# Kernel tuning notes

Hardware: AMD Instinct MI355X
Metric: run time of the kernel (lower is better)

Reference implementation:

```python
import jax, jax.numpy as jnp
import numpy as np

EPS = 1e-5

def fwht(x):
    """Normalized fast Walsh-Hadamard transform along the last axis (len must be power of 2)."""
    orig_shape = x.shape
    n = orig_shape[-1]
    x = x.reshape(-1, n)
    h = 1
    while h < n:
        x = x.reshape(-1, n // (2 * h), 2, h)
        a, b = x[:, :, 0, :], x[:, :, 1, :]
        x = jnp.stack([a + b, a - b], axis=2).reshape(-1, n)
        h *= 2
    return (x * (1.0 / np.sqrt(n))).reshape(orig_shape)

def act_quant(x):
    """Per-token 8-bit absmax activation quantization (BitNet), with STE identity."""
    scale = 127.0 / jnp.clip(jnp.max(jnp.abs(x), axis=-1, keepdims=True), EPS)
    q = jnp.clip(jnp.round(x * scale), -128.0, 127.0) / scale
    return x + jax.lax.stop_gradient(q - x)

def weight_quant(w):
    """Ternary (1.58-bit) absmean weight quantization (BitNet b1.58), with STE identity."""
    scale = jnp.clip(jnp.mean(jnp.abs(w)), EPS)
    q = jnp.clip(jnp.round(w / scale), -1.0, 1.0) * scale
    return w + jax.lax.stop_gradient(q - w)

def h_bitlinear(x, w):
    """EnhancedHBitLinear: Hadamard-rotate activations, quantize acts+weights, matmul."""
    xq = act_quant(fwht(x))
    wq = weight_quant(w)
    return jnp.einsum('bsh,oh->bso', xq, wq)

def setup_inputs() -> dict:
    key = jax.random.key(0)
    k1, k2, k3, k4 = jax.random.split(key, 4)
    H, I = 2048, 8192
    B, S = 2, 2048
    hidden_states = jax.random.normal(k1, (B, S, H), dtype=jnp.float32)
    w_gate = jax.random.normal(k2, (I, H), dtype=jnp.float32) * 0.02
    w_up = jax.random.normal(k3, (I, H), dtype=jnp.float32) * 0.02
    w_down = jax.random.normal(k4, (H, I), dtype=jnp.float32) * 0.02
    return {"hidden_states": hidden_states, "w_gate": w_gate, "w_up": w_up, "w_down": w_down}

def reference(hidden_states, w_gate, w_up, w_down):
    gate = h_bitlinear(hidden_states, w_gate)          # [B,S,I]
    up = h_bitlinear(hidden_states, w_up)              # [B,S,I]
    return h_bitlinear(jax.nn.silu(gate) * up, w_down)  # [B,S,H]
```

## Files before the change

### kernel.cpp

```cpp
#include <hip/hip_runtime.h>
#include <math.h>

#define EPSF 1e-5f

typedef __attribute__((ext_vector_type(4))) int i32x4;

#define S_WAITCNT_VMCNT(N) asm volatile("s_waitcnt vmcnt(" #N ")" ::: "memory")
#define S_WAITCNT_LGKM0() asm volatile("s_waitcnt lgkmcnt(0)" ::: "memory")

__device__ __forceinline__ void gload_lds16(const void* g, void* l) {
  __builtin_amdgcn_global_load_lds(
      (const __attribute__((address_space(1))) void*)g,
      (__attribute__((address_space(3))) void*)l, 16, 0, 0);
}

__global__ void zero_sums_kernel(double* sums) {
  if (threadIdx.x < 3) sums[threadIdx.x] = 0.0;
}

__global__ __launch_bounds__(256) void absmean_kernel(
    const float* __restrict__ wg, const float* __restrict__ wu,
    const float* __restrict__ wd, double* __restrict__ sums) {
  const int N4 = 16777216 / 4;
  const float* W = (blockIdx.y == 0) ? wg : ((blockIdx.y == 1) ? wu : wd);
  double acc = 0.0;
  const int stride = gridDim.x * 256;
  for (int i = blockIdx.x * 256 + threadIdx.x; i < N4; i += stride) {
    float4 v = ((const float4*)W)[i];
    acc += (double)fabsf(v.x);
    acc += (double)fabsf(v.y);
    acc += (double)fabsf(v.z);
    acc += (double)fabsf(v.w);
  }
  for (int o = 32; o > 0; o >>= 1) acc += __shfl_down(acc, o);
  __shared__ double sred[4];
  const int wid = threadIdx.x >> 6, lane = threadIdx.x & 63;
  if (lane == 0) sred[wid] = acc;
  __syncthreads();
  if (threadIdx.x == 0)
    atomicAdd(&sums[blockIdx.y], sred[0] + sred[1] + sred[2] + sred[3]);
}

__global__ __launch_bounds__(256) void wquant_kernel(
    const float* __restrict__ wg, const float* __restrict__ wu,
    const float* __restrict__ wd, signed char* __restrict__ qg,
    signed char* __restrict__ qu, signed char* __restrict__ qd,
    const double* __restrict__ sums, float* __restrict__ scalef) {
  const int mat = blockIdx.y;
  const float* W = (mat == 0) ? wg : ((mat == 1) ? wu : wd);
  signed char* Q = (mat == 0) ? qg : ((mat == 1) ? qu : qd);
  const float scale = fmaxf((float)(sums[mat] * (1.0 / 16777216.0)), EPSF);
  if (blockIdx.x == 0 && threadIdx.x == 0) scalef[mat] = scale;
  const int i = blockIdx.x * 256 + threadIdx.x;
  float4 v = ((const float4*)W)[i];
  int q0 = (int)fminf(fmaxf(rintf(v.x / scale), -1.f), 1.f);
  int q1 = (int)fminf(fmaxf(rintf(v.y / scale), -1.f), 1.f);
  int q2 = (int)fminf(fmaxf(rintf(v.z / scale), -1.f), 1.f);
  int q3 = (int)fminf(fmaxf(rintf(v.w / scale), -1.f), 1.f);
  int packed = (q0 & 0xff) | ((q1 & 0xff) << 8) | ((q2 & 0xff) << 16) | (q3 << 24);
  ((int*)Q)[i] = packed;
}

template <int N>
__global__ __launch_bounds__(256) void fwht_quant_kernel(
    const float* __restrict__ X, signed char* __restrict__ Q,
    float* __restrict__ drow, float cnorm) {
  __shared__ float s[N];
  __shared__ float red[4];
  const int tid = threadIdx.x;
  const size_t row = blockIdx.x;
  const float* x = X + row * (size_t)N;
  for (int i = tid; i < N / 4; i += 256)
    ((float4*)s)[i] = ((const float4*)x)[i];
  __syncthreads();
  for (int h = 1; h < N; h <<= 1) {
    for (int p = tid; p < N / 2; p += 256) {
      int i = ((p & ~(h - 1)) << 1) | (p & (h - 1));
      int j = i + h;
      float a = s[i], b = s[j];
      s[i] = a + b;
      s[j] = a - b;
    }
    __syncthreads();
  }
  const int PER = N / 256;
  float m = 0.f;
  for (int i = tid * PER; i < tid * PER + PER; ++i) m = fmaxf(m, fabsf(s[i]));
  for (int o = 32; o > 0; o >>= 1) m = fmaxf(m, __shfl_xor(m, o));
  const int wid = tid >> 6, lane = tid & 63;
  if (lane == 0) red[wid] = m;
  __syncthreads();
  m = fmaxf(fmaxf(red[0], red[1]), fmaxf(red[2], red[3]));
  const float maxv = fmaxf(m * cnorm, EPSF);
  const float scale = 127.0f / maxv;
  if (tid == 0) drow[row] = maxv / 127.0f;
  const size_t qbase = row * (size_t)N + (size_t)tid * PER;
#pragma unroll
  for (int i0 = 0; i0 < PER; i0 += 4) {
    int q[4];
#pragma unroll
    for (int k = 0; k < 4; ++k) {
      float y = s[tid * PER + i0 + k] * cnorm;
      float qf = rintf(y * scale);
      qf = fminf(fmaxf(qf, -128.f), 127.f);
      q[k] = (int)qf;
    }
    int packed =
        (q[0] & 0xff) | ((q[1] & 0xff) << 8) | ((q[2] & 0xff) << 16) | (q[3] << 24);
    *(int*)(Q + qbase + i0) = packed;
  }
}

__global__ __launch_bounds__(256, 2) void gemm1_kernel(
    const signed char* __restrict__ Aq, const signed char* __restrict__ Bg,
    const signed char* __restrict__ Bu, const float* __restrict__ drow,
    const float* __restrict__ scalef, float* __restrict__ H) {
  const int K = 2048, T = K / 64;
  const int BUF = 24576;
  __shared__ __align__(16) signed char smem[3 * BUF];
  const int tid = threadIdx.x;
  const int wid = tid >> 6;
  const int lane = tid & 63;
  const int wr = wid >> 1, wc = wid & 1;

  const int orig = blockIdx.y * 64 + blockIdx.x;
  const int swz = (orig & 7) * 256 + (orig >> 3);
  const int mbase = (swz >> 6) * 128, nbase = (swz & 63) * 128;

  const int srow = tid >> 2;
  const int scol = (((tid & 3) ^ ((srow >> 1) & 3)) << 4);
  const signed char* gA = Aq + (size_t)(mbase + srow) * K + scol;
  const signed char* gG = Bg + (size_t)(nbase + srow) * K + scol;
  const signed char* gU = Bu + (size_t)(nbase + srow) * K + scol;

  i32x4 accG[4][4] = {};
  i32x4 accU[4][4] = {};

  auto stage = [&](int boff, int kk) {
    const size_t o = (size_t)kk;
    const int lb = boff + (wid << 10);
    gload_lds16(gA + o, &smem[lb]);
    gload_lds16(gA + o + (size_t)64 * K, &smem[lb + 4096]);
    gload_lds16(gG + o, &smem[lb + 8192]);
    gload_lds16(gG + o + (size_t)64 * K, &smem[lb + 12288]);
    gload_lds16(gU + o, &smem[lb + 16384]);
    gload_lds16(gU + o + (size_t)64 * K, &smem[lb + 20480]);
  };

  const int kos = (((lane >> 4) ^ ((lane >> 1) & 3)) << 4);
  const int rA = (wr << 6) + (lane & 15);
  const int rB = (wc << 6) + (lane & 15);

  stage(0, 0);
  stage(BUF, 64);
  int bc = 0, bn = BUF, bf = 2 * BUF;
  for (int t = 0; t < T; ++t) {
    S_WAITCNT_VMCNT(6);
    __builtin_amdgcn_s_barrier();
    __builtin_amdgcn_sched_barrier(0);
    const int kk = (t + 2 < T) ? (t + 2) * 64 : (T - 1) * 64;
    stage(bf, kk);
    i32x4 a[4], bg[4], bu[4];
#pragma unroll
    for (int m = 0; m < 4; ++m)
      a[m] = *(const i32x4*)&smem[bc + (rA + m * 16) * 64 + kos];
#pragma unroll
    for (int n = 0; n < 4; ++n) {
      bg[n] = *(const i32x4*)&smem[bc + 8192 + (rB + n * 16) * 64 + kos];
      bu[n] = *(const i32x4*)&smem[bc + 16384 + (rB + n * 16) * 64 + kos];
    }
    __builtin_amdgcn_s_setprio(1);
#pragma unroll
    for (int m = 0; m < 4; ++m)
#pragma unroll
      for (int n = 0; n < 4; ++n) {
        accG[m][n] =
            __builtin_amdgcn_mfma_i32_16x16x64_i8(a[m], bg[n], accG[m][n], 0, 0, 0);
        accU[m][n] =
            __builtin_amdgcn_mfma_i32_16x16x64_i8(a[m], bu[n], accU[m][n], 0, 0, 0);
      }
    __builtin_amdgcn_s_setprio(0);
    S_WAITCNT_LGKM0();
    __builtin_amdgcn_sched_barrier(0);
    const int tmp = bc; bc = bn; bn = bf; bf = tmp;
  }

  const float sg = scalef[0], su = scalef[1];
  const int orow = (lane >> 4) << 2;
  const int ocol = lane & 15;
#pragma unroll
  for (int m = 0; m < 4; ++m)
#pragma unroll
    for (int n = 0; n < 4; ++n)
#pragma unroll
      for (int j = 0; j < 4; ++j) {
        int grow = mbase + (wr << 6) + m * 16 + orow + j;
        int gcol = nbase + (wc << 6) + n * 16 + ocol;
        float dr = drow[grow];
        float gate = (float)accG[m][n][j] * (sg * dr);
        float up = (float)accU[m][n][j] * (su * dr);
        float hval = (gate / (1.0f + expf(-gate))) * up;
        H[(size_t)grow * 8192 + gcol] = hval;
      }
}

__global__ __launch_bounds__(256, 3) void gemm2_kernel(
    const signed char* __restrict__ Aq, const signed char* __restrict__ Bq,
    const float* __restrict__ drow, const float* __restrict__ scalef,
    float* __restrict__ O) {
  const int K = 8192, T = K / 64;
  const int BUF = 16384;
  __shared__ __align__(16) signed char smem[3 * BUF];
  const int tid = threadIdx.x;
  const int wid = tid >> 6;
  const int lane = tid & 63;
  const int wr = wid >> 1, wc = wid & 1;

  const int orig = blockIdx.y * 16 + blockIdx.x;
  const int swz = (orig & 7) * 64 + (orig >> 3);
  const int mbase = (swz >> 4) * 128, nbase = (swz & 15) * 128;

  const int srow = tid >> 2;
  const int scol = (((tid & 3) ^ ((srow >> 1) & 3)) << 4);
  const signed char* gA = Aq + (size_t)(mbase + srow) * K + scol;
  const signed char* gB = Bq + (size_t)(nbase + srow) * K + scol;

  i32x4 acc[4][4] = {};

  auto stage = [&](int boff, int kk) {
    const size_t o = (size_t)kk;
    const int lb = boff + (wid << 10);
    gload_lds16(gA + o, &smem[lb]);
    gload_lds16(gA + o + (size_t)64 * K, &smem[lb + 4096]);
    gload_lds16(gB + o, &smem[lb + 8192]);
    gload_lds16(gB + o + (size_t)64 * K, &smem[lb + 12288]);
  };

  const int kos = (((lane >> 4) ^ ((lane >> 1) & 3)) << 4);
  const int rA = (wr << 6) + (lane & 15);
  const int rB = (wc << 6) + (lane & 15);

  stage(0, 0);
  stage(BUF, 64);
  int bc = 0, bn = BUF, bf = 2 * BUF;
  for (int t = 0; t < T; ++t) {
    S_WAITCNT_VMCNT(4);
    __builtin_amdgcn_s_barrier();
    __builtin_amdgcn_sched_barrier(0);
    const int kk = (t + 2 < T) ? (t + 2) * 64 : (T - 1) * 64;
    stage(bf, kk);
    i32x4 a[4], b[4];
#pragma unroll
    for (int m = 0; m < 4; ++m)
      a[m] = *(const i32x4*)&smem[bc + (rA + m * 16) * 64 + kos];
#pragma unroll
    for (int n = 0; n < 4; ++n)
      b[n] = *(const i32x4*)&smem[bc + 8192 + (rB + n * 16) * 64 + kos];
    __builtin_amdgcn_s_setprio(1);
#pragma unroll
    for (int m = 0; m < 4; ++m)
#pragma unroll
      for (int n = 0; n < 4; ++n)
        acc[m][n] = __builtin_amdgcn_mfma_i32_16x16x64_i8(a[m], b[n], acc[m][n], 0, 0, 0);
    __builtin_amdgcn_s_setprio(0);
    S_WAITCNT_LGKM0();
    __builtin_amdgcn_sched_barrier(0);
    const int tmp = bc; bc = bn; bn = bf; bf = tmp;
  }

  const float sd = scalef[2];
  const int orow = (lane >> 4) << 2;
  const int ocol = lane & 15;
#pragma unroll
  for (int m = 0; m < 4; ++m)
#pragma unroll
    for (int n = 0; n < 4; ++n)
#pragma unroll
      for (int j = 0; j < 4; ++j) {
        int grow = mbase + (wr << 6) + m * 16 + orow + j;
        int gcol = nbase + (wc << 6) + n * 16 + ocol;
        O[(size_t)grow * 2048 + gcol] = (float)acc[m][n][j] * (sd * drow[grow]);
      }
}

extern "C" void kernel_launch(void* const* d_in, const int* in_sizes, int n_in,
                              void* d_out, int out_size, void* d_ws, size_t ws_size,
                              hipStream_t stream) {
  (void)in_sizes; (void)n_in; (void)out_size; (void)ws_size;
  const float* x = (const float*)d_in[0];
  const float* wg = (const float*)d_in[1];
  const float* wu = (const float*)d_in[2];
  const float* wd = (const float*)d_in[3];
  float* out = (float*)d_out;

  char* ws = (char*)d_ws;
  double* sums = (double*)ws;
  float* scalef = (float*)(ws + 256);
  size_t off = 1024;
  signed char* qg = (signed char*)(ws + off); off += 16777216;
  signed char* qu = (signed char*)(ws + off); off += 16777216;
  signed char* qd = (signed char*)(ws + off); off += 16777216;
  signed char* xq = (signed char*)(ws + off); off += 8388608;
  signed char* hq = (signed char*)(ws + off); off += 33554432;
  float* dr1 = (float*)(ws + off); off += 16384;
  float* dr2 = (float*)(ws + off); off += 16384;
  float* Hbuf = (float*)(ws + off); off += (size_t)4096 * 8192 * 4;

  zero_sums_kernel<<<1, 64, 0, stream>>>(sums);
  absmean_kernel<<<dim3(1024, 3), 256, 0, stream>>>(wg, wu, wd, sums);
  wquant_kernel<<<dim3(16384, 3), 256, 0, stream>>>(wg, wu, wd, qg, qu, qd, sums,
                                                    scalef);
  const float c1 = (float)(1.0 / sqrt(2048.0));
  const float c2 = (float)(1.0 / sqrt(8192.0));
  fwht_quant_kernel<2048><<<4096, 256, 0, stream>>>(x, xq, dr1, c1);
  gemm1_kernel<<<dim3(64, 32), 256, 0, stream>>>(xq, qg, qu, dr1, scalef, Hbuf);
  fwht_quant_kernel<8192><<<4096, 256, 0, stream>>>(Hbuf, hq, dr2, c2);
  gemm2_kernel<<<dim3(16, 32), 256, 0, stream>>>(hq, qd, dr2, scalef, out);
}
```

Baseline: 630.6 us.

## Use 256x128 tiles with 8 waves, split-phase pipelining and XCD-aware tile mapping

Both int8 GEMMs move from 128x128 tiles with 4 waves to 256x128 tiles with 8 waves (512 threads). Each K-step is split into two halves, with global-to-LDS prefetch loads and extra barriers interleaved between the MFMA groups. Block indices are remapped so that tiles sharing B columns stay on the same XCD, which is meant to improve L2 reuse. The cost is fewer blocks (256 for gemm2) and extra barriers per iteration, which may lower occupancy and latency hiding.

```diff
diff --git a/kernel.cpp b/kernel.cpp
--- a/kernel.cpp
+++ b/kernel.cpp
@@ -111,160 +111,190 @@
   }
 }
 
-__global__ __launch_bounds__(256, 2) void gemm1_kernel(
+__global__ __launch_bounds__(512, 2) void gemm1_kernel(
     const signed char* __restrict__ Aq, const signed char* __restrict__ Bg,
     const signed char* __restrict__ Bu, const float* __restrict__ drow,
     const float* __restrict__ scalef, float* __restrict__ H) {
   const int K = 2048, T = K / 64;
+  const int BUF = 32768;
+  __shared__ __align__(16) signed char smem[3 * BUF];
+  const int tid = threadIdx.x;
+  const int wid = tid >> 6;
+  const int lane = tid & 63;
+  const int wr = wid >> 2, wn = wid & 3;
+
+  const int id = blockIdx.x;
+  const int xcd = id & 7, j = id >> 3;
+  const int mbase = (j & 15) * 256;
+  const int nbase = (xcd * 8 + (j >> 4)) * 128;
+
+  const int srow = tid >> 2;
+  const int scol = (((tid & 3) ^ ((srow >> 1) & 3)) << 4);
+  const signed char* pA = Aq + (size_t)(mbase + srow) * K + scol;
+  const signed char* pG = Bg + (size_t)(nbase + srow) * K + scol;
+  const signed char* pU = Bu + (size_t)(nbase + srow) * K + scol;
+
+  i32x4 accG[8][2] = {};
+  i32x4 accU[8][2] = {};
+
+  const int kos = (((lane >> 4) ^ ((lane >> 1) & 3)) << 4);
+  const int rA = (wr << 7) + (lane & 15);
+  const int rB = (wn << 5) + (lane & 15);
+
+  const int wb = wid << 10;
+
+  {
+    gload_lds16(pA, &smem[wb]);
+    gload_lds16(pA + (size_t)128 * K, &smem[8192 + wb]);
+    gload_lds16(pG, &smem[16384 + wb]);
+    gload_lds16(pU, &smem[24576 + wb]);
+    gload_lds16(pA + 64, &smem[BUF + wb]);
+    gload_lds16(pA + (size_t)128 * K + 64, &smem[BUF + 8192 + wb]);
+    gload_lds16(pG + 64, &smem[BUF + 16384 + wb]);
+    gload_lds16(pU + 64, &smem[BUF + 24576 + wb]);
+  }
+
+  int bc = 0, bn = BUF, bf = 2 * BUF;
+  for (int t = 0; t < T; ++t) {
+    const size_t kk = (size_t)((t + 2 < T) ? (t + 2) * 64 : (T - 1) * 64);
+    S_WAITCNT_VMCNT(4);
+    __builtin_amdgcn_s_barrier();
+    __builtin_amdgcn_sched_barrier(0);
+    i32x4 a[8], bg[2], bu[2];
+#pragma unroll
+    for (int m = 0; m < 8; ++m)
+      a[m] = *(const i32x4*)&smem[bc + (rA + m * 16) * 64 + kos];
+#pragma unroll
+    for (int n = 0; n < 2; ++n)
+      bg[n] = *(const i32x4*)&smem[bc + 16384 + (rB + n * 16) * 64 + kos];
+    gload_lds16(pA + kk, &smem[bf + wb]);
+    gload_lds16(pA + (size_t)128 * K + kk, &smem[bf + 8192 + wb]);
+    __builtin_amdgcn_s_barrier();
+    S_WAITCNT_LGKM0();
+    __builtin_amdgcn_sched_barrier(0);
+    __builtin_amdgcn_s_setprio(1);
+#pragma unroll
+    for (int m = 0; m < 8; ++m)
+#pragma unroll
+      for (int n = 0; n < 2; ++n)
+        accG[m][n] =
+            __builtin_amdgcn_mfma_i32_16x16x64_i8(a[m], bg[n], accG[m][n], 0, 0, 0);
+    __builtin_amdgcn_s_setprio(0);
+#pragma unroll
+    for (int n = 0; n < 2; ++n)
+      bu[n] = *(const i32x4*)&smem[bc + 24576 + (rB + n * 16) * 64 + kos];
+    gload_lds16(pG + kk, &smem[bf + 16384 + wb]);
+    gload_lds16(pU + kk, &smem[bf + 24576 + wb]);
+    __builtin_amdgcn_s_barrier();
+    S_WAITCNT_LGKM0();
+    __builtin_amdgcn_sched_barrier(0);
+    __builtin_amdgcn_s_setprio(1);
+#pragma unroll
+    for (int m = 0; m < 8; ++m)
+#pragma unroll
+      for (int n = 0; n < 2; ++n)
+        accU[m][n] =
+            __builtin_amdgcn_mfma_i32_16x16x64_i8(a[m], bu[n], accU[m][n], 0, 0, 0);
+    __builtin_amdgcn_s_setprio(0);
+    const int tmp = bc; bc = bn; bn = bf; bf = tmp;
+  }
+
+  const float sg = scalef[0], su = scalef[1];
+  const int orow = (lane >> 4) << 2;
+  const int ocol = lane & 15;
+#pragma unroll
+  for (int m = 0; m < 8; ++m)
+#pragma unroll
+    for (int n = 0; n < 2; ++n)
+#pragma unroll
+      for (int jj = 0; jj < 4; ++jj) {
+        int grow = mbase + (wr << 7) + m * 16 + orow + jj;
+        int gcol = nbase + (wn << 5) + n * 16 + ocol;
+        float dr = drow[grow];
+        float gate = (float)accG[m][n][jj] * (sg * dr);
+        float up = (float)accU[m][n][jj] * (su * dr);
+        float hval = (gate / (1.0f + expf(-gate))) * up;
+        H[(size_t)grow * 8192 + gcol] = hval;
+      }
+}
+
+__global__ __launch_bounds__(512, 2) void gemm2_kernel(
+    const signed char* __restrict__ Aq, const signed char* __restrict__ Bq,
+    const float* __restrict__ drow, const float* __restrict__ scalef,
+    float* __restrict__ O) {
+  const int K = 8192, T = K / 64;
   const int BUF = 24576;
   __shared__ __align__(16) signed char smem[3 * BUF];
   const int tid = threadIdx.x;
   const int wid = tid >> 6;
   const int lane = tid & 63;
-  const int wr = wid >> 1, wc = wid & 1;
-
-  const int orig = blockIdx.y * 64 + blockIdx.x;
-  const int swz = (orig & 7) * 256 + (orig >> 3);
-  const int mbase = (swz >> 6) * 128, nbase = (swz & 63) * 128;
+  const int wr = wid >> 2, wn = wid & 3;
+
+  const int id = blockIdx.x;
+  const int xcd = id & 7, j = id >> 3;
+  const int mbase = (j & 15) * 256;
+  const int nbase = (xcd * 2 + (j >> 4)) * 128;
 
   const int srow = tid >> 2;
   const int scol = (((tid & 3) ^ ((srow >> 1) & 3)) << 4);
-  const signed char* gA = Aq + (size_t)(mbase + srow) * K + scol;
-  const signed char* gG = Bg + (size_t)(nbase + srow) * K + scol;
-  const signed char* gU = Bu + (size_t)(nbase + srow) * K + scol;
-
-  i32x4 accG[4][4] = {};
-  i32x4 accU[4][4] = {};
-
-  auto stage = [&](int boff, int kk) {
-    const size_t o = (size_t)kk;
-    const int lb = boff + (wid << 10);
-    gload_lds16(gA + o, &smem[lb]);
-    gload_lds16(gA + o + (size_t)64 * K, &smem[lb + 4096]);
-    gload_lds16(gG + o, &smem[lb + 8192]);
-    gload_lds16(gG + o + (size_t)64 * K, &smem[lb + 12288]);
-    gload_lds16(gU + o, &smem[lb + 16384]);
-    gload_lds16(gU + o + (size_t)64 * K, &smem[lb + 20480]);
-  };
+  const signed char* pA = Aq + (size_t)(mbase + srow) * K + scol;
+  const signed char* pB = Bq + (size_t)(nbase + srow) * K + scol;
+
+  i32x4 acc[8][2] = {};
 
   const int kos = (((lane >> 4) ^ ((lane >> 1) & 3)) << 4);
-  const int rA = (wr << 6) + (lane & 15);
-  const int rB = (wc << 6) + (lane & 15);
-
-  stage(0, 0);
-  stage(BUF, 64);
+  const int rA = (wr << 7) + (lane & 15);
+  const int rB = (wn << 5) + (lane & 15);
+  const int wb = wid << 10;
+
+  {
+    gload_lds16(pA, &smem[wb]);
+    gload_lds16(pA + (size_t)128 * K, &smem[8192 + wb]);
+    gload_lds16(pB, &smem[16384 + wb]);
+    gload_lds16(pA + 64, &smem[BUF + wb]);
+    gload_lds16(pA + (size_t)128 * K + 64, &smem[BUF + 8192 + wb]);
+    gload_lds16(pB + 64, &smem[BUF + 16384 + wb]);
+  }
+
   int bc = 0, bn = BUF, bf = 2 * BUF;
   for (int t = 0; t < T; ++t) {
-    S_WAITCNT_VMCNT(6);
-    __builtin_amdgcn_s_barrier();
-    __builtin_amdgcn_sched_barrier(0);
-    const int kk = (t + 2 < T) ? (t + 2) * 64 : (T - 1) * 64;
-    stage(bf, kk);
-    i32x4 a[4], bg[4], bu[4];
+    const size_t kk = (size_t)((t + 2 < T) ? (t + 2) * 64 : (T - 1) * 64);
+    S_WAITCNT_VMCNT(3);
+    __builtin_amdgcn_s_barrier();
+    __builtin_amdgcn_sched_barrier(0);
+    i32x4 a[8], b[2];
 #pragma unroll
     for (int m = 0; m < 4; ++m)
       a[m] = *(const i32x4*)&smem[bc + (rA + m * 16) * 64 + kos];
 #pragma unroll
-    for (int n = 0; n < 4; ++n) {
-      bg[n] = *(const i32x4*)&smem[bc + 8192 + (rB + n * 16) * 64 + kos];
-      bu[n] = *(const i32x4*)&smem[bc + 16384 + (rB + n * 16) * 64 + kos];
-    }
+    for (int n = 0; n < 2; ++n)
+      b[n] = *(const i32x4*)&smem[bc + 16384 + (rB + n * 16) * 64 + kos];
+    gload_lds16(pA + kk, &smem[bf + wb]);
+    gload_lds16(pA + (size_t)128 * K + kk, &smem[bf + 8192 + wb]);
+    __builtin_amdgcn_s_barrier();
+    S_WAITCNT_LGKM0();
+    __builtin_amdgcn_sched_barrier(0);
     __builtin_amdgcn_s_setprio(1);
 #pragma unroll
     for (int m = 0; m < 4; ++m)
 #pragma unroll
-      for (int n = 0; n < 4; ++n) {
-        accG[m][n] =
-            __builtin_amdgcn_mfma_i32_16x16x64_i8(a[m], bg[n], accG[m][n], 0, 0, 0);
-        accU[m][n] =
-            __builtin_amdgcn_mfma_i32_16x16x64_i8(a[m], bu[n], accU[m][n], 0, 0, 0);
-      }
-    __builtin_amdgcn_s_setprio(0);
-    S_WAITCNT_LGKM0();
-    __builtin_amdgcn_sched_barrier(0);
-    const int tmp = bc; bc = bn; bn = bf; bf = tmp;
-  }
-
-  const float sg = scalef[0], su = scalef[1];
-  const int orow = (lane >> 4) << 2;
-  const int ocol = lane & 15;
-#pragma unroll
-  for (int m = 0; m < 4; ++m)
-#pragma unroll
-    for (int n = 0; n < 4; ++n)
-#pragma unroll
-      for (int j = 0; j < 4; ++j) {
-        int grow = mbase + (wr << 6) + m * 16 + orow + j;
-        int gcol = nbase + (wc << 6) + n * 16 + ocol;
-        float dr = drow[grow];
-        float gate = (float)accG[m][n][j] * (sg * dr);
-        float up = (float)accU[m][n][j] * (su * dr);
-        float hval = (gate / (1.0f + expf(-gate))) * up;
-        H[(size_t)grow * 8192 + gcol] = hval;
-      }
-}
-
-__global__ __launch_bounds__(256, 3) void gemm2_kernel(
-    const signed char* __restrict__ Aq, const signed char* __restrict__ Bq,
-    const float* __restrict__ drow, const float* __restrict__ scalef,
-    float* __restrict__ O) {
-  const int K = 8192, T = K / 64;
-  const int BUF = 16384;
-  __shared__ __align__(16) signed char smem[3 * BUF];
-  const int tid = threadIdx.x;
-  const int wid = tid >> 6;
-  const int lane = tid & 63;
-  const int wr = wid >> 1, wc = wid & 1;
-
-  const int orig = blockIdx.y * 16 + blockIdx.x;
-  const int swz = (orig & 7) * 64 + (orig >> 3);
-  const int mbase = (swz >> 4) * 128, nbase = (swz & 15) * 128;
-
-  const int srow = tid >> 2;
-  const int scol = (((tid & 3) ^ ((srow >> 1) & 3)) << 4);
-  const signed char* gA = Aq + (size_t)(mbase + srow) * K + scol;
-  const signed char* gB = Bq + (size_t)(nbase + srow) * K + scol;
-
-  i32x4 acc[4][4] = {};
-
-  auto stage = [&](int boff, int kk) {
-    const size_t o = (size_t)kk;
-    const int lb = boff + (wid << 10);
-    gload_lds16(gA + o, &smem[lb]);
-    gload_lds16(gA + o + (size_t)64 * K, &smem[lb + 4096]);
-    gload_lds16(gB + o, &smem[lb + 8192]);
-    gload_lds16(gB + o + (size_t)64 * K, &smem[lb + 12288]);
-  };
-
-  const int kos = (((lane >> 4) ^ ((lane >> 1) & 3)) << 4);
-  const int rA = (wr << 6) + (lane & 15);
-  const int rB = (wc << 6) + (lane & 15);
-
-  stage(0, 0);
-  stage(BUF, 64);
-  int bc = 0, bn = BUF, bf = 2 * BUF;
-  for (int t = 0; t < T; ++t) {
-    S_WAITCNT_VMCNT(4);
-    __builtin_amdgcn_s_barrier();
-    __builtin_amdgcn_sched_barrier(0);
-    const int kk = (t + 2 < T) ? (t + 2) * 64 : (T - 1) * 64;
-    stage(bf, kk);
-    i32x4 a[4], b[4];
-#pragma unroll
-    for (int m = 0; m < 4; ++m)
-      a[m] = *(const i32x4*)&smem[bc + (rA + m * 16) * 64 + kos];
-#pragma unroll
-    for (int n = 0; n < 4; ++n)
-      b[n] = *(const i32x4*)&smem[bc + 8192 + (rB + n * 16) * 64 + kos];
-    __builtin_amdgcn_s_setprio(1);
-#pragma unroll
-    for (int m = 0; m < 4; ++m)
-#pragma unroll
-      for (int n = 0; n < 4; ++n)
+      for (int n = 0; n < 2; ++n)
         acc[m][n] = __builtin_amdgcn_mfma_i32_16x16x64_i8(a[m], b[n], acc[m][n], 0, 0, 0);
     __builtin_amdgcn_s_setprio(0);
+#pragma unroll
+    for (int m = 4; m < 8; ++m)
+      a[m] = *(const i32x4*)&smem[bc + (rA + m * 16) * 64 + kos];
+    gload_lds16(pB + kk, &smem[bf + 16384 + wb]);
+    __builtin_amdgcn_s_barrier();
     S_WAITCNT_LGKM0();
     __builtin_amdgcn_sched_barrier(0);
+    __builtin_amdgcn_s_setprio(1);
+#pragma unroll
+    for (int m = 4; m < 8; ++m)
+#pragma unroll
+      for (int n = 0; n < 2; ++n)
+        acc[m][n] = __builtin_amdgcn_mfma_i32_16x16x64_i8(a[m], b[n], acc[m][n], 0, 0, 0);
+    __builtin_amdgcn_s_setprio(0);
     const int tmp = bc; bc = bn; bn = bf; bf = tmp;
   }
 
@@ -272,14 +302,14 @@
   const int orow = (lane >> 4) << 2;
   const int ocol = lane & 15;
 #pragma unroll
-  for (int m = 0; m < 4; ++m)
-#pragma unroll
-    for (int n = 0; n < 4; ++n)
-#pragma unroll
-      for (int j = 0; j < 4; ++j) {
-        int grow = mbase + (wr << 6) + m * 16 + orow + j;
-        int gcol = nbase + (wc << 6) + n * 16 + ocol;
-        O[(size_t)grow * 2048 + gcol] = (float)acc[m][n][j] * (sd * drow[grow]);
+  for (int m = 0; m < 8; ++m)
+#pragma unroll
+    for (int n = 0; n < 2; ++n)
+#pragma unroll
+      for (int jj = 0; jj < 4; ++jj) {
+        int grow = mbase + (wr << 7) + m * 16 + orow + jj;
+        int gcol = nbase + (wn << 5) + n * 16 + ocol;
+        O[(size_t)grow * 2048 + gcol] = (float)acc[m][n][jj] * (sd * drow[grow]);
       }
 }
 
@@ -313,7 +343,7 @@
   const float c1 = (float)(1.0 / sqrt(2048.0));
   const float c2 = (float)(1.0 / sqrt(8192.0));
   fwht_quant_kernel<2048><<<4096, 256, 0, stream>>>(x, xq, dr1, c1);
-  gemm1_kernel<<<dim3(64, 32), 256, 0, stream>>>(xq, qg, qu, dr1, scalef, Hbuf);
+  gemm1_kernel<<<1024, 512, 0, stream>>>(xq, qg, qu, dr1, scalef, Hbuf);
   fwht_quant_kernel<8192><<<4096, 256, 0, stream>>>(Hbuf, hq, dr2, c2);
-  gemm2_kernel<<<dim3(16, 32), 256, 0, stream>>>(hq, qd, dr2, scalef, out);
-}
+  gemm2_kernel<<<256, 512, 0, stream>>>(hq, qd, dr2, scalef, out);
+}
```

New measurement: 610.8 us. -3.1%, faster.
